# Performance work log

Measured on AMD Instinct MI355X. Metric: run time of the kernel, lower is better.

## Reference

```python
import jax, jax.numpy as jnp
import numpy as np

T, B, H = 2048, 64, 1024


def setup_inputs() -> dict:
    key = jax.random.key(0)
    k1, k2, k3 = jax.random.split(key, 3)
    hidden = jax.random.normal(k1, (1, B, H), dtype=jnp.float32)
    encoder_outputs = jax.random.normal(k2, (T, B, H), dtype=jnp.float32)
    W_attn = jax.random.normal(k3, (H, H), dtype=jnp.float32) * (1.0 / np.sqrt(H))
    b_attn = jnp.zeros((H,), dtype=jnp.float32)
    return {"hidden": hidden, "encoder_outputs": encoder_outputs,
            "W_attn": W_attn, "b_attn": b_attn}


def reference(hidden, encoder_outputs, W_attn, b_attn):
    # 'general' scoring: energy_tb = hidden_b . (W @ enc_tb + b)
    proj = jnp.einsum('tbh,gh->tbg', encoder_outputs, W_attn) + b_attn  # [T,B,H]
    scores = jnp.einsum('bh,tbh->bt', hidden[0], proj)                  # [B,T]
    attn = jax.nn.softmax(scores, axis=1)
    return attn[:, None, :]  # [B,1,T]
```

## Files before the change

### kernel.cpp

```cpp
#include <hip/hip_runtime.h>
#include <math.h>

#define T_DIM 2048
#define B_DIM 64
#define H_DIM 1024
#define TC 16

typedef float f4 __attribute__((ext_vector_type(4)));

__global__ __launch_bounds__(512) void qproj_kernel(
    const float* __restrict__ hidden,
    const float* __restrict__ W,
    float* __restrict__ q) {
    const int b0   = blockIdx.y * 4;
    const int h0   = blockIdx.x * 256;
    const int wave = threadIdx.x >> 6;
    const int lane = threadIdx.x & 63;

    __shared__ float hs[4][H_DIM];
    __shared__ f4    part[8][4][64];

    for (int i = threadIdx.x; i < 4 * H_DIM; i += 512)
        hs[i >> 10][i & 1023] = hidden[(size_t)b0 * H_DIM + i];
    __syncthreads();

    const int gbase = wave * 128;
    const f4* Wv = (const f4*)(W + (size_t)gbase * H_DIM + h0);
    f4 acc0 = {0,0,0,0}, acc1 = {0,0,0,0}, acc2 = {0,0,0,0}, acc3 = {0,0,0,0};
#pragma unroll 4
    for (int g = 0; g < 128; ++g) {
        const f4 wv = Wv[g * 256 + lane];
        acc0 += hs[0][gbase + g] * wv;
        acc1 += hs[1][gbase + g] * wv;
        acc2 += hs[2][gbase + g] * wv;
        acc3 += hs[3][gbase + g] * wv;
    }
    part[wave][0][lane] = acc0;
    part[wave][1][lane] = acc1;
    part[wave][2][lane] = acc2;
    part[wave][3][lane] = acc3;
    __syncthreads();

    if (wave < 4) {
        f4 s = part[0][wave][lane];
#pragma unroll
        for (int w = 1; w < 8; ++w) s += part[w][wave][lane];
        ((f4*)(q + (size_t)(b0 + wave) * H_DIM + h0))[lane] = s;
    }
}

__global__ __launch_bounds__(512) void scores_kernel(
    const float* __restrict__ enc,
    const float* __restrict__ q,
    float* __restrict__ scores) {
    const int wave = threadIdx.x >> 6;
    const int lane = threadIdx.x & 63;
    const int t0   = blockIdx.x * TC;
    const int b0   = blockIdx.y * 16 + wave * 2;

    f4 qf0[4], qf1[4];
    {
        const f4* qv0 = (const f4*)(q + (size_t)b0 * H_DIM);
        const f4* qv1 = (const f4*)(q + (size_t)(b0 + 1) * H_DIM);
#pragma unroll
        for (int k = 0; k < 4; ++k) {
            qf0[k] = qv0[k * 64 + lane];
            qf1[k] = qv1[k * 64 + lane];
        }
    }

#pragma unroll 2
    for (int tt = 0; tt < TC; ++tt) {
        const int t = t0 + tt;
        const f4* e0p = (const f4*)(enc + ((size_t)t * B_DIM + b0) * H_DIM);
        const f4* e1p = e0p + 256;

        f4 E0[4], E1[4];
#pragma unroll
        for (int k = 0; k < 4; ++k)
            E0[k] = __builtin_nontemporal_load(&e0p[k * 64 + lane]);
#pragma unroll
        for (int k = 0; k < 4; ++k)
            E1[k] = __builtin_nontemporal_load(&e1p[k * 64 + lane]);

        float a0 = 0.f, a1 = 0.f;
#pragma unroll
        for (int k = 0; k < 4; ++k) {
            a0 += E0[k].x * qf0[k].x + E0[k].y * qf0[k].y +
                  E0[k].z * qf0[k].z + E0[k].w * qf0[k].w;
            a1 += E1[k].x * qf1[k].x + E1[k].y * qf1[k].y +
                  E1[k].z * qf1[k].z + E1[k].w * qf1[k].w;
        }

        const bool odd = lane & 1;
        float m = odd ? a1 : a0;
        float o = odd ? a0 : a1;
        m += __shfl_xor(o, 1);
#pragma unroll
        for (int off = 2; off < 64; off <<= 1)
            m += __shfl_xor(m, off);

        if (lane < 2)
            scores[(size_t)(b0 + lane) * T_DIM + t] = m;
    }
}

__global__ __launch_bounds__(512) void softmax_kernel(
    const float* __restrict__ scores,
    float* __restrict__ out) {
    const int b    = blockIdx.x;
    const int tid  = threadIdx.x;
    const int wave = tid >> 6;
    const int lane = tid & 63;

    f4 v = ((const f4*)(scores + (size_t)b * T_DIM))[tid];

    float m = fmaxf(fmaxf(v.x, v.y), fmaxf(v.z, v.w));
#pragma unroll
    for (int off = 1; off < 64; off <<= 1)
        m = fmaxf(m, __shfl_xor(m, off));

    __shared__ float redm[8], reds[8];
    if (lane == 0) redm[wave] = m;
    __syncthreads();
    m = redm[0];
#pragma unroll
    for (int w = 1; w < 8; ++w) m = fmaxf(m, redm[w]);

    v.x = expf(v.x - m); v.y = expf(v.y - m);
    v.z = expf(v.z - m); v.w = expf(v.w - m);
    float s = v.x + v.y + v.z + v.w;
#pragma unroll
    for (int off = 1; off < 64; off <<= 1)
        s += __shfl_xor(s, off);
    if (lane == 0) reds[wave] = s;
    __syncthreads();
    s = reds[0];
#pragma unroll
    for (int w = 1; w < 8; ++w) s += reds[w];

    const float inv = 1.0f / s;
    v *= inv;
    ((f4*)(out + (size_t)b * T_DIM))[tid] = v;
}

extern "C" void kernel_launch(void* const* d_in, const int* in_sizes, int n_in,
                              void* d_out, int out_size, void* d_ws, size_t ws_size,
                              hipStream_t stream) {
    const float* hidden = (const float*)d_in[0];
    const float* enc    = (const float*)d_in[1];
    const float* W      = (const float*)d_in[2];

    float* out    = (float*)d_out;
    float* q      = (float*)d_ws;
    float* scores = (float*)d_ws + (size_t)B_DIM * H_DIM;

    qproj_kernel  <<<dim3(H_DIM / 256, B_DIM / 4), 512, 0, stream>>>(hidden, W, q);
    scores_kernel <<<dim3(T_DIM / TC, B_DIM / 16), 512, 0, stream>>>(enc, q, scores);
    softmax_kernel<<<dim3(B_DIM),                  512, 0, stream>>>(scores, out);
}
```

Baseline: 98.50 us.

## Fuse softmax into scores kernel via last-block atomic counter per batch group

Removes the separate softmax launch. Each scores block increments a per-batch-group counter after a threadfence, and the last block to finish in each group runs the softmax over its 16 batch rows. The counters are reset inside qproj_kernel. This saves one kernel launch and its gap, but the tail softmax now runs on only 4 blocks serially over 16 rows each, instead of 64 blocks in parallel.

```diff
diff --git a/kernel.cpp b/kernel.cpp
--- a/kernel.cpp
+++ b/kernel.cpp
@@ -11,7 +11,11 @@
 __global__ __launch_bounds__(512) void qproj_kernel(
     const float* __restrict__ hidden,
     const float* __restrict__ W,
-    float* __restrict__ q) {
+    float* __restrict__ q,
+    int* __restrict__ counters) {
+    if (blockIdx.x == 0 && blockIdx.y == 0 && threadIdx.x < 4)
+        counters[threadIdx.x] = 0;
+
     const int b0   = blockIdx.y * 4;
     const int h0   = blockIdx.x * 256;
     const int wave = threadIdx.x >> 6;
@@ -49,14 +53,17 @@
     }
 }
 
-__global__ __launch_bounds__(512) void scores_kernel(
+__global__ __launch_bounds__(512) void scores_softmax_kernel(
     const float* __restrict__ enc,
     const float* __restrict__ q,
-    float* __restrict__ scores) {
+    float* __restrict__ scores,
+    int* __restrict__ counters,
+    float* __restrict__ out) {
     const int wave = threadIdx.x >> 6;
     const int lane = threadIdx.x & 63;
+    const int y    = blockIdx.y;
     const int t0   = blockIdx.x * TC;
-    const int b0   = blockIdx.y * 16 + wave * 2;
+    const int b0   = y * 16 + wave * 2;
 
     f4 qf0[4], qf1[4];
     {
@@ -103,45 +110,47 @@
         if (lane < 2)
             scores[(size_t)(b0 + lane) * T_DIM + t] = m;
     }
-}
 
-__global__ __launch_bounds__(512) void softmax_kernel(
-    const float* __restrict__ scores,
-    float* __restrict__ out) {
-    const int b    = blockIdx.x;
-    const int tid  = threadIdx.x;
-    const int wave = tid >> 6;
-    const int lane = tid & 63;
-
-    f4 v = ((const f4*)(scores + (size_t)b * T_DIM))[tid];
-
-    float m = fmaxf(fmaxf(v.x, v.y), fmaxf(v.z, v.w));
-#pragma unroll
-    for (int off = 1; off < 64; off <<= 1)
-        m = fmaxf(m, __shfl_xor(m, off));
+    __threadfence();
+    __shared__ int done;
+    if (threadIdx.x == 0) done = atomicAdd(&counters[y], 1);
+    __syncthreads();
+    if (done != gridDim.x - 1) return;
+    __threadfence();
 
     __shared__ float redm[8], reds[8];
-    if (lane == 0) redm[wave] = m;
-    __syncthreads();
-    m = redm[0];
+    const int tid = threadIdx.x;
+    for (int r = 0; r < 16; ++r) {
+        const int b = y * 16 + r;
+        f4 v = ((const f4*)(scores + (size_t)b * T_DIM))[tid];
+
+        float m = fmaxf(fmaxf(v.x, v.y), fmaxf(v.z, v.w));
 #pragma unroll
-    for (int w = 1; w < 8; ++w) m = fmaxf(m, redm[w]);
+        for (int off = 1; off < 64; off <<= 1)
+            m = fmaxf(m, __shfl_xor(m, off));
+        if (lane == 0) redm[wave] = m;
+        __syncthreads();
+        m = redm[0];
+#pragma unroll
+        for (int w = 1; w < 8; ++w) m = fmaxf(m, redm[w]);
 
-    v.x = expf(v.x - m); v.y = expf(v.y - m);
-    v.z = expf(v.z - m); v.w = expf(v.w - m);
-    float s = v.x + v.y + v.z + v.w;
+        v.x = expf(v.x - m); v.y = expf(v.y - m);
+        v.z = expf(v.z - m); v.w = expf(v.w - m);
+        float s = v.x + v.y + v.z + v.w;
 #pragma unroll
-    for (int off = 1; off < 64; off <<= 1)
-        s += __shfl_xor(s, off);
-    if (lane == 0) reds[wave] = s;
-    __syncthreads();
-    s = reds[0];
+        for (int off = 1; off < 64; off <<= 1)
+            s += __shfl_xor(s, off);
+        if (lane == 0) reds[wave] = s;
+        __syncthreads();
+        s = reds[0];
 #pragma unroll
-    for (int w = 1; w < 8; ++w) s += reds[w];
+        for (int w = 1; w < 8; ++w) s += reds[w];
 
-    const float inv = 1.0f / s;
-    v *= inv;
-    ((f4*)(out + (size_t)b * T_DIM))[tid] = v;
+        const float inv = 1.0f / s;
+        v *= inv;
+        ((f4*)(out + (size_t)b * T_DIM))[tid] = v;
+        __syncthreads();
+    }
 }
 
 extern "C" void kernel_launch(void* const* d_in, const int* in_sizes, int n_in,
@@ -151,11 +160,13 @@
     const float* enc    = (const float*)d_in[1];
     const float* W      = (const float*)d_in[2];
 
-    float* out    = (float*)d_out;
-    float* q      = (float*)d_ws;
-    float* scores = (float*)d_ws + (size_t)B_DIM * H_DIM;
+    float* out      = (float*)d_out;
+    float* q        = (float*)d_ws;
+    float* scores   = (float*)d_ws + (size_t)B_DIM * H_DIM;
+    int*   counters = (int*)(scores + (size_t)B_DIM * T_DIM);
 
-    qproj_kernel  <<<dim3(H_DIM / 256, B_DIM / 4), 512, 0, stream>>>(hidden, W, q);
-    scores_kernel <<<dim3(T_DIM / TC, B_DIM / 16), 512, 0, stream>>>(enc, q, scores);
-    softmax_kernel<<<dim3(B_DIM),                  512, 0, stream>>>(scores, out);
+    qproj_kernel<<<dim3(H_DIM / 256, B_DIM / 4), 512, 0, stream>>>(
+        hidden, W, q, counters);
+    scores_softmax_kernel<<<dim3(T_DIM / TC, B_DIM / 16), 512, 0, stream>>>(
+        enc, q, scores, counters, out);
 }
```

Result: slower. 307.7 us (+212.4%).
